# Performance work log

Measured on AMD Instinct MI355X. Metric: run time of the kernel, lower is better.

Reference implementation:

```python
import jax, jax.numpy as jnp
import numpy as np

INPUT_DIM = 64
HIDDEN_DIM = 512
DIM_INNER = int(HIDDEN_DIM * 1.5)  # 768


def log_g(x):
    # torch.where(x >= 0, (relu(x) + 0.5).log(), -softplus(-x))
    return jnp.where(x >= 0, jnp.log(jax.nn.relu(x) + 0.5), -jax.nn.softplus(-x))


def setup_inputs() -> dict:
    key = jax.random.key(0)
    k_x, k1, k2, k3, k4 = jax.random.split(key, 5)
    B, S = 16, 4096
    x = jax.random.normal(k_x, (B, S, INPUT_DIM), dtype=jnp.float32)
    # weights stored as [in, out] (transpose of torch Linear.weight); bias=False everywhere
    W_in = jax.random.normal(k1, (INPUT_DIM, HIDDEN_DIM), dtype=jnp.float32) * 0.02
    W_hg = jax.random.normal(k2, (HIDDEN_DIM, 2 * DIM_INNER), dtype=jnp.float32) * 0.02
    W_out = jax.random.normal(k3, (DIM_INNER, HIDDEN_DIM), dtype=jnp.float32) * 0.02
    W_final = jax.random.normal(k4, (HIDDEN_DIM, 1), dtype=jnp.float32) * 0.02
    return {"x": x, "W_in": W_in, "W_hg": W_hg, "W_out": W_out, "W_final": W_final}


def reference(x, W_in, W_hg, W_out, W_final):
    # x: [B, S, input_dim]
    h = jnp.einsum('bsi,ih->bsh', x, W_in)                 # [B,S,H]
    hg = jnp.einsum('bsh,hd->bsd', h, W_hg)                # [B,S,2*DI]
    hidden, gate = jnp.split(hg, 2, axis=-1)               # each [B,S,DI]
    # seq_len > 1 path, prev_hidden=None
    log_coeffs = -jax.nn.softplus(gate)                    # log(1 - z)
    log_z = -jax.nn.softplus(-gate)                        # log(z)
    log_values = log_z + log_g(hidden)
    # heinsen associative scan in log space
    a_star = jnp.cumsum(log_coeffs, axis=1)
    log_h = a_star + jax.lax.cumlogsumexp(log_values - a_star, axis=1)
    out = jnp.exp(log_h)                                   # [B,S,DI]
    out = jnp.einsum('bsd,dh->bsh', out, W_out)            # [B,S,H]
    predictions = jnp.einsum('bsh,ho->bso', out, W_final)[..., 0]  # [B,S]
    return predictions
```

## Files before the change

kernel.cpp:

```cpp
#include <hip/hip_runtime.h>
#include <hip/hip_fp16.h>

typedef unsigned short u16;
typedef unsigned int   u32;
typedef __bf16 bf16x8 __attribute__((ext_vector_type(8)));
typedef float  f32x4  __attribute__((ext_vector_type(4)));

constexpr int BB   = 16;
constexpr int S    = 4096;
constexpr int M    = BB * S;
constexpr int DIN  = 64;
constexpr int H    = 512;
constexpr int DI   = 768;
constexpr int N2   = 1536;
constexpr int CL   = 128;
constexpr int NCHUNK = M / CL;
constexpr int NSEG  = NCHUNK * 4;
constexpr int SEGB  = S / 32;
constexpr int DTILES = 12;

constexpr size_t OFF_XB    = 0;
constexpr size_t OFF_B2C   = 8388608;
constexpr size_t OFF_WC    = 8585216;
constexpr size_t OFF_SEGC  = 8589312;
constexpr size_t OFF_SEGVH = 14880768;
constexpr size_t OFF_PART  = 21172224;

constexpr float L2E = 1.4426950408889634f;

__device__ __forceinline__ u16 f2bf(float f) {
  u32 u = __float_as_uint(f);
  u32 r = (u + 0x7FFFu + ((u >> 16) & 1u)) >> 16;
  return (u16)r;
}

__device__ __forceinline__ int cvs(int row, int d) {
  return row * 64 + (d ^ (((row >> 2) & 3) << 4));
}

__global__ __launch_bounds__(256) void prep_xb(const float* __restrict__ x,
                                               u16* __restrict__ xb) {
  size_t i = (size_t)(blockIdx.x * 256 + threadIdx.x) * 8;
  float4 f0 = *(const float4*)(x + i);
  float4 f1 = *(const float4*)(x + i + 4);
  u32 w0 = f2bf(f0.x) | ((u32)f2bf(f0.y) << 16);
  u32 w1 = f2bf(f0.z) | ((u32)f2bf(f0.w) << 16);
  u32 w2 = f2bf(f1.x) | ((u32)f2bf(f1.y) << 16);
  u32 w3 = f2bf(f1.z) | ((u32)f2bf(f1.w) << 16);
  uint4 o = make_uint4(w0, w1, w2, w3);
  *(uint4*)(xb + i) = o;
}

__global__ __launch_bounds__(256) void prep_b2c(const float* __restrict__ Win,
                                                const float* __restrict__ Whg,
                                                u16* __restrict__ B2c) {
  __shared__ float Wl[64][65];
  const int tid = threadIdx.x;
  const int k = tid & 63;
  const int nloc = tid >> 6;
  const int n = blockIdx.x * 4 + nloc;
  const int g = n >> 5, r = n & 31;
  const int col = (r < 16) ? (g * 16 + r) : (DI + g * 16 + (r - 16));
  float acc = 0.f;
  for (int jc = 0; jc < H; jc += 64) {
    const int jl = tid & 63, k0 = tid >> 6;
    #pragma unroll
    for (int s = 0; s < 16; ++s) {
      int kr = k0 + 4 * s;
      Wl[kr][jl] = Win[kr * H + jc + jl];
    }
    __syncthreads();
    #pragma unroll 8
    for (int j = 0; j < 64; ++j)
      acc = fmaf(Wl[k][j], Whg[(size_t)(jc + j) * N2 + col], acc);
    __syncthreads();
  }
  B2c[n * 64 + k] = f2bf(acc);
}

__global__ __launch_bounds__(256) void prep_wcomb(const float* __restrict__ Wout,
                                                  const float* __restrict__ Wfin,
                                                  float* __restrict__ wc) {
  int wv = threadIdx.x >> 6, ln = threadIdx.x & 63;
  int d = blockIdx.x * 4 + wv;
  const float* row = Wout + (size_t)d * H;
  float s = 0.f;
  #pragma unroll
  for (int j = 0; j < 8; ++j) {
    int k = j * 64 + ln;
    s += row[k] * Wfin[k];
  }
  #pragma unroll
  for (int off = 32; off; off >>= 1) s += __shfl_xor(s, off);
  if (ln == 0) wc[d] = s;
}

template<int PASS>
__global__ __launch_bounds__(256) void fused_gemm_scan(
    const u16* __restrict__ xb, const u16* __restrict__ B2c,
    const float* __restrict__ Hin, const float* __restrict__ wcomb,
    float* __restrict__ SegC, float* __restrict__ SegV,
    float* __restrict__ part) {
  __shared__ __align__(16) u16 AB[16384];
  u32* cvl = (u32*)AB;

  const int tid = threadIdx.x, wv = tid >> 6, ln = tid & 63;
  const int nt = blockIdx.x % DTILES, ck = blockIdx.x / DTILES;
  const int m0 = ck * CL;
  const int wr = wv >> 1, wcol = wv & 1;
  const int lrow = ln & 15, hi4 = ln >> 4;

  {
    const uint4* gA = (const uint4*)(xb + (size_t)m0 * 64);
    const uint4* gB = (const uint4*)(B2c + (size_t)nt * 128 * 64);
    uint4* lA = (uint4*)AB;
    uint4* lB = (uint4*)(AB + 8192);
    #pragma unroll
    for (int j = 0; j < 4; ++j) {
      int q = j * 256 + tid;
      int qs = (q & ~7) | ((q & 7) ^ ((q >> 3) & 7));
      lA[qs] = gA[q];
      lB[qs] = gB[q];
    }
  }
  __syncthreads();

  f32x4 acc[4][4] = {};
  {
    const u16* Al = AB;
    const u16* Bl = AB + 8192;
    #pragma unroll
    for (int kk = 0; kk < 2; ++kk) {
      bf16x8 af[4], bfr[4];
      #pragma unroll
      for (int i = 0; i < 4; ++i) {
        int row = wr * 64 + i * 16 + lrow;
        af[i] = *(const bf16x8*)&Al[row * 64 + (((kk * 4 + hi4) ^ (row & 7)) << 3)];
      }
      #pragma unroll
      for (int j = 0; j < 4; ++j) {
        int row = wcol * 64 + j * 16 + lrow;
        bfr[j] = *(const bf16x8*)&Bl[row * 64 + (((kk * 4 + hi4) ^ (row & 7)) << 3)];
      }
      #pragma unroll
      for (int i = 0; i < 4; ++i)
        #pragma unroll
        for (int j = 0; j < 4; ++j)
          acc[i][j] = __builtin_amdgcn_mfma_f32_16x16x32_bf16(af[i], bfr[j], acc[i][j], 0, 0, 0);
    }
  }
  __syncthreads();

  #pragma unroll
  for (int i = 0; i < 4; ++i)
    #pragma unroll
    for (int jp = 0; jp < 2; ++jp) {
      f32x4 hid = acc[i][2 * jp + 0];
      f32x4 gat = acc[i][2 * jp + 1];
      const int dl = (wcol * 2 + jp) * 16 + lrow;
      #pragma unroll
      for (int r = 0; r < 4; ++r) {
        int row = wr * 64 + i * 16 + hi4 * 4 + r;
        float gate = gat[r], hidden = hid[r];
        float eg  = __builtin_amdgcn_exp2f(gate * L2E);
        float cc  = __builtin_amdgcn_rcpf(1.0f + eg);
        float zz  = eg * cc;
        float gneg = __builtin_amdgcn_rcpf(
                        1.0f + __builtin_amdgcn_exp2f(-hidden * L2E));
        float gg  = (hidden >= 0.0f) ? (hidden + 0.5f) : gneg;
        float vv  = zz * gg;
        __half2 p = __floats2half2_rn(cc, vv);
        cvl[cvs(row, dl)] = *(const u32*)&p;
      }
    }
  __syncthreads();

  const int seg = ck * 4 + wv;
  if (PASS == 1) {
    float Cp = 1.f, Vp = 0.f;
    #pragma unroll 8
    for (int tt = 0; tt < 32; ++tt) {
      u32 u = cvl[cvs(wv * 32 + tt, ln)];
      __half2 hv = *(const __half2*)&u;
      float c = __half2float(__low2half(hv));
      float v = __half2float(__high2half(hv));
      Vp = fmaf(c, Vp, v);
      Cp *= c;
    }
    SegC[(size_t)seg * DI + nt * 64 + ln] = Cp;
    SegV[(size_t)seg * DI + nt * 64 + ln] = Vp;
  } else {
    float h = Hin[(size_t)seg * DI + nt * 64 + ln];
    const float wd = wcomb[nt * 64 + ln];
    #pragma unroll 4
    for (int tt = 0; tt < 32; ++tt) {
      const int t = wv * 32 + tt;
      u32 u = cvl[cvs(t, ln)];
      __half2 hv = *(const __half2*)&u;
      float c = __half2float(__low2half(hv));
      float v = __half2float(__high2half(hv));
      h = fmaf(c, h, v);
      float pv = h * wd;
      cvl[t * 64 + ((ln + t) & 63)] = __float_as_uint(pv);
    }
    __syncthreads();
    const int row = tid >> 1, half = tid & 1;
    float s = 0.f;
    #pragma unroll 8
    for (int jj = 0; jj < 32; ++jj) {
      int idx = (half * 32 + jj + row) & 63;
      s += __uint_as_float(cvl[row * 64 + idx]);
    }
    s += __shfl_xor(s, 1);
    if (half == 0) part[(size_t)nt * M + m0 + row] = s;
  }
}

__global__ __launch_bounds__(768) void scan_carry(const float* __restrict__ SegC,
                                                  float* __restrict__ SegVH) {
  const int b = blockIdx.x, d = threadIdx.x;
  float carry = 0.f;
  for (int q = 0; q < SEGB; ++q) {
    size_t idx = (size_t)(b * SEGB + q) * DI + d;
    float tmp = fmaf(SegC[idx], carry, SegVH[idx]);
    SegVH[idx] = carry;
    carry = tmp;
  }
}

__global__ __launch_bounds__(256) void reduce12(const float* __restrict__ part,
                                                float* __restrict__ out) {
  int i = blockIdx.x * 256 + threadIdx.x;
  float s = 0.f;
  #pragma unroll
  for (int w = 0; w < DTILES; ++w) s += part[(size_t)w * M + i];
  out[i] = s;
}

extern "C" void kernel_launch(void* const* d_in, const int* in_sizes, int n_in,
                              void* d_out, int out_size, void* d_ws, size_t ws_size,
                              hipStream_t stream) {
  const float* x    = (const float*)d_in[0];
  const float* Win  = (const float*)d_in[1];
  const float* Whg  = (const float*)d_in[2];
  const float* Wout = (const float*)d_in[3];
  const float* Wfin = (const float*)d_in[4];
  float* out = (float*)d_out;
  char* ws = (char*)d_ws;

  u16*   xb    = (u16*)(ws + OFF_XB);
  u16*   B2c   = (u16*)(ws + OFF_B2C);
  float* wc    = (float*)(ws + OFF_WC);
  float* SegC  = (float*)(ws + OFF_SEGC);
  float* SegVH = (float*)(ws + OFF_SEGVH);
  float* part  = (float*)(ws + OFF_PART);

  prep_xb   <<<2048, 256, 0, stream>>>(x, xb);
  prep_b2c  <<<384,  256, 0, stream>>>(Win, Whg, B2c);
  prep_wcomb<<<192,  256, 0, stream>>>(Wout, Wfin, wc);
  fused_gemm_scan<1><<<NCHUNK * DTILES, 256, 0, stream>>>(xb, B2c, SegVH, wc, SegC, SegVH, part);
  scan_carry<<<BB, DI, 0, stream>>>(SegC, SegVH);
  fused_gemm_scan<2><<<NCHUNK * DTILES, 256, 0, stream>>>(xb, B2c, SegVH, wc, SegC, SegVH, part);
  reduce12  <<<256,  256, 0, stream>>>(part, out);
}
```

Measured before the change: 151.6 us.

## Compute pass-1 segment summaries in registers via shuffles; parallelize carry scan

```diff
diff --git a/kernel.cpp b/kernel.cpp
--- a/kernel.cpp
+++ b/kernel.cpp
@@ -15,7 +15,6 @@
 constexpr int N2   = 1536;
 constexpr int CL   = 128;
 constexpr int NCHUNK = M / CL;
-constexpr int NSEG  = NCHUNK * 4;
 constexpr int SEGB  = S / 32;
 constexpr int DTILES = 12;
 
@@ -36,6 +35,25 @@
 
 __device__ __forceinline__ int cvs(int row, int d) {
   return row * 64 + (d ^ (((row >> 2) & 3) << 4));
+}
+
+__device__ __forceinline__ void act_cv(float hidden, float gate,
+                                       float& cc, float& vv) {
+  float eg  = __builtin_amdgcn_exp2f(gate * L2E);
+  cc = __builtin_amdgcn_rcpf(1.0f + eg);
+  float zz  = eg * cc;
+  float gneg = __builtin_amdgcn_rcpf(
+                  1.0f + __builtin_amdgcn_exp2f(-hidden * L2E));
+  float gg  = (hidden >= 0.0f) ? (hidden + 0.5f) : gneg;
+  vv = zz * gg;
+}
+
+__device__ __forceinline__ void comb_step(float& C, float& V, int bit, int ln) {
+  float Cp = __shfl_xor(C, bit);
+  float Vp = __shfl_xor(V, bit);
+  bool up = (ln & bit) != 0;
+  V = up ? fmaf(C, Vp, V) : fmaf(Cp, V, Vp);
+  C *= Cp;
 }
 
 __global__ __launch_bounds__(256) void prep_xb(const float* __restrict__ x,
@@ -149,57 +167,68 @@
           acc[i][j] = __builtin_amdgcn_mfma_f32_16x16x32_bf16(af[i], bfr[j], acc[i][j], 0, 0, 0);
     }
   }
-  __syncthreads();
-
-  #pragma unroll
-  for (int i = 0; i < 4; ++i)
+
+  if (PASS == 1) {
     #pragma unroll
     for (int jp = 0; jp < 2; ++jp) {
-      f32x4 hid = acc[i][2 * jp + 0];
-      f32x4 gat = acc[i][2 * jp + 1];
-      const int dl = (wcol * 2 + jp) * 16 + lrow;
-      #pragma unroll
-      for (int r = 0; r < 4; ++r) {
-        int row = wr * 64 + i * 16 + hi4 * 4 + r;
-        float gate = gat[r], hidden = hid[r];
-        float eg  = __builtin_amdgcn_exp2f(gate * L2E);
-        float cc  = __builtin_amdgcn_rcpf(1.0f + eg);
-        float zz  = eg * cc;
-        float gneg = __builtin_amdgcn_rcpf(
-                        1.0f + __builtin_amdgcn_exp2f(-hidden * L2E));
-        float gg  = (hidden >= 0.0f) ? (hidden + 0.5f) : gneg;
-        float vv  = zz * gg;
-        __half2 p = __floats2half2_rn(cc, vv);
-        cvl[cvs(row, dl)] = *(const u32*)&p;
+      const int d = nt * 64 + (wcol * 2 + jp) * 16 + lrow;
+      #pragma unroll
+      for (int sl = 0; sl < 2; ++sl) {
+        float Cr[2], Vr[2];
+        #pragma unroll
+        for (int ii = 0; ii < 2; ++ii) {
+          const int i = sl * 2 + ii;
+          float C = 1.f, V = 0.f;
+          #pragma unroll
+          for (int r = 0; r < 4; ++r) {
+            float cc, vvv;
+            act_cv(acc[i][2 * jp + 0][r], acc[i][2 * jp + 1][r], cc, vvv);
+            V = fmaf(cc, V, vvv);
+            C *= cc;
+          }
+          comb_step(C, V, 16, ln);
+          comb_step(C, V, 32, ln);
+          Cr[ii] = C; Vr[ii] = V;
+        }
+        float Cs = Cr[0] * Cr[1];
+        float Vs = fmaf(Cr[1], Vr[0], Vr[1]);
+        if (hi4 == 0) {
+          int seg = ck * 4 + wr * 2 + sl;
+          SegC[(size_t)seg * DI + d] = Cs;
+          SegV[(size_t)seg * DI + d] = Vs;
+        }
       }
     }
-  __syncthreads();
-
-  const int seg = ck * 4 + wv;
-  if (PASS == 1) {
-    float Cp = 1.f, Vp = 0.f;
-    #pragma unroll 8
-    for (int tt = 0; tt < 32; ++tt) {
-      u32 u = cvl[cvs(wv * 32 + tt, ln)];
-      __half2 hv = *(const __half2*)&u;
-      float c = __half2float(__low2half(hv));
-      float v = __half2float(__high2half(hv));
-      Vp = fmaf(c, Vp, v);
-      Cp *= c;
-    }
-    SegC[(size_t)seg * DI + nt * 64 + ln] = Cp;
-    SegV[(size_t)seg * DI + nt * 64 + ln] = Vp;
   } else {
+    __syncthreads();
+
+    #pragma unroll
+    for (int i = 0; i < 4; ++i)
+      #pragma unroll
+      for (int jp = 0; jp < 2; ++jp) {
+        const int dl = (wcol * 2 + jp) * 16 + lrow;
+        #pragma unroll
+        for (int r = 0; r < 4; ++r) {
+          int row = wr * 64 + i * 16 + hi4 * 4 + r;
+          float cc, vvv;
+          act_cv(acc[i][2 * jp + 0][r], acc[i][2 * jp + 1][r], cc, vvv);
+          __half2 p = __floats2half2_rn(cc, vvv);
+          cvl[cvs(row, dl)] = *(const u32*)&p;
+        }
+      }
+    __syncthreads();
+
+    const int seg = ck * 4 + wv;
     float h = Hin[(size_t)seg * DI + nt * 64 + ln];
     const float wd = wcomb[nt * 64 + ln];
     #pragma unroll 4
     for (int tt = 0; tt < 32; ++tt) {
       const int t = wv * 32 + tt;
       u32 u = cvl[cvs(t, ln)];
-      __half2 hv = *(const __half2*)&u;
-      float c = __half2float(__low2half(hv));
-      float v = __half2float(__high2half(hv));
-      h = fmaf(c, h, v);
+      float hn;
+      asm("v_fma_mix_f32 %0, %1, %2, %1 op_sel:[0,0,1] op_sel_hi:[1,0,1]"
+          : "=v"(hn) : "v"(u), "v"(h));
+      h = hn;
       float pv = h * wd;
       cvl[t * 64 + ((ln + t) & 63)] = __float_as_uint(pv);
     }
@@ -216,15 +245,26 @@
   }
 }
 
-__global__ __launch_bounds__(768) void scan_carry(const float* __restrict__ SegC,
+__global__ __launch_bounds__(128) void scan_carry(const float* __restrict__ SegC,
                                                   float* __restrict__ SegVH) {
-  const int b = blockIdx.x, d = threadIdx.x;
+  const int b = blockIdx.x / 6, dc = blockIdx.x % 6;
+  const int d = dc * 128 + threadIdx.x;
+  const size_t base = (size_t)b * SEGB * DI + d;
   float carry = 0.f;
-  for (int q = 0; q < SEGB; ++q) {
-    size_t idx = (size_t)(b * SEGB + q) * DI + d;
-    float tmp = fmaf(SegC[idx], carry, SegVH[idx]);
-    SegVH[idx] = carry;
-    carry = tmp;
+  for (int q0 = 0; q0 < SEGB; q0 += 16) {
+    float c16[16], v16[16];
+    #pragma unroll
+    for (int j = 0; j < 16; ++j) {
+      size_t idx = base + (size_t)(q0 + j) * DI;
+      c16[j] = SegC[idx];
+      v16[j] = SegVH[idx];
+    }
+    #pragma unroll
+    for (int j = 0; j < 16; ++j) {
+      size_t idx = base + (size_t)(q0 + j) * DI;
+      SegVH[idx] = carry;
+      carry = fmaf(c16[j], carry, v16[j]);
+    }
   }
 }
 
@@ -259,7 +299,7 @@
   prep_b2c  <<<384,  256, 0, stream>>>(Win, Whg, B2c);
   prep_wcomb<<<192,  256, 0, stream>>>(Wout, Wfin, wc);
   fused_gemm_scan<1><<<NCHUNK * DTILES, 256, 0, stream>>>(xb, B2c, SegVH, wc, SegC, SegVH, part);
-  scan_carry<<<BB, DI, 0, stream>>>(SegC, SegVH);
+  scan_carry<<<96, 128, 0, stream>>>(SegC, SegVH);
   fused_gemm_scan<2><<<NCHUNK * DTILES, 256, 0, stream>>>(xb, B2c, SegVH, wc, SegC, SegVH, part);
   reduce12  <<<256,  256, 0, stream>>>(part, out);
 }
```

Measured after the change: 137.4 us. -9.3%, faster.
